# Kernel optimization log

Hardware: AMD Instinct MI355X
Metric: run time of the kernel (lower is better)

## Reference

```python
import jax, jax.numpy as jnp
import numpy as np

TOP_K = 8
N_EXPERTS = 64
ALPHA = 0.1
NORM_TOPK = True
SEQ_AUX = True


def setup_inputs() -> dict:
    key = jax.random.key(0)
    k1, k2 = jax.random.split(key)
    B, S, H = 4, 4096, 2048
    hidden_states = jax.random.normal(k1, (B, S, H), dtype=jnp.float32)
    # kaiming_uniform_(a=sqrt(5)) => bound = 1/sqrt(fan_in)
    bound = 1.0 / np.sqrt(H)
    weight = jax.random.uniform(k2, (N_EXPERTS, H), dtype=jnp.float32,
                                minval=-bound, maxval=bound)
    return {"hidden_states": hidden_states, "weight": weight}


def reference(hidden_states, weight):
    B, S, H = hidden_states.shape
    E, K = N_EXPERTS, TOP_K
    x = hidden_states.reshape(-1, H)                 # [T, H], T = B*S
    logits = jnp.einsum('th,eh->te', x, weight)      # gating GEMM
    scores = jax.nn.softmax(logits, axis=-1)         # [T, E]
    topk_weight, topk_idx = jax.lax.top_k(scores, K) # [T, K]
    if K > 1 and NORM_TOPK:
        topk_weight = topk_weight / (topk_weight.sum(-1, keepdims=True) + 1e-20)

    # batch-level load stats (bincount over selections)
    expert_loads = jnp.zeros((E,), jnp.float32).at[topk_idx.reshape(-1)].add(1.0)

    # sequence-level auxiliary load-balancing loss
    if SEQ_AUX:
        idx_b = topk_idx.reshape(B, S * K)           # [B, S*K]
        ce = jnp.zeros((B, E), jnp.float32)
        ce = ce.at[jnp.arange(B)[:, None], idx_b].add(1.0)
        ce = ce / (S * K / E)
        mean_scores = scores.reshape(B, S, E).mean(axis=1)   # [B, E]
        aux_loss = (ce * mean_scores).sum(axis=1).mean() * ALPHA
    else:
        ce = jax.nn.one_hot(topk_idx.reshape(-1), E).mean(0)
        Pi = scores.mean(0)
        aux_loss = (Pi * ce * E).sum() * ALPHA

    return (topk_idx, topk_weight, aux_loss, expert_loads)
```

## Files before the change

### kernel.cpp

```cpp
#include <hip/hip_runtime.h>
#include <hip/hip_bf16.h>
#include <math.h>

#define TOK 16384
#define HDIM 2048
#define NE 64
#define NB 4
#define KTOP 8
#define KC 64
#define NC (HDIM / KC)
#define BT 32

typedef __attribute__((ext_vector_type(8))) __bf16 bf16x8;
typedef __attribute__((ext_vector_type(4))) float f32x4;
typedef unsigned int uint;

__device__ __forceinline__ uint asu(float f) { union { float f; uint u; } c; c.f = f; return c.u; }
__device__ __forceinline__ float asf(uint u) { union { uint u; float f; } c; c.u = u; return c.f; }

__device__ __forceinline__ void split3(float v, uint& h, uint& m, uint& l) {
  uint u = asu(v);
  h = u & 0xffff0000u;
  float d = v - asf(h);
  m = asu(d) & 0xffff0000u;
  float d2 = d - asf(m);
  l = asu(d2);
}

__device__ __forceinline__ void split8(float4 a, float4 b,
                                       bf16x8& h8, bf16x8& m8, bf16x8& l8) {
  union { uint4 u; bf16x8 v; } H, M, L;
  uint h0, m0, l0, h1, m1, l1;
  split3(a.x, h0, m0, l0); split3(a.y, h1, m1, l1);
  H.u.x = (h0 >> 16) | (h1 & 0xffff0000u);
  M.u.x = (m0 >> 16) | (m1 & 0xffff0000u);
  L.u.x = (l0 >> 16) | (l1 & 0xffff0000u);
  split3(a.z, h0, m0, l0); split3(a.w, h1, m1, l1);
  H.u.y = (h0 >> 16) | (h1 & 0xffff0000u);
  M.u.y = (m0 >> 16) | (m1 & 0xffff0000u);
  L.u.y = (l0 >> 16) | (l1 & 0xffff0000u);
  split3(b.x, h0, m0, l0); split3(b.y, h1, m1, l1);
  H.u.z = (h0 >> 16) | (h1 & 0xffff0000u);
  M.u.z = (m0 >> 16) | (m1 & 0xffff0000u);
  L.u.z = (l0 >> 16) | (l1 & 0xffff0000u);
  split3(b.z, h0, m0, l0); split3(b.w, h1, m1, l1);
  H.u.w = (h0 >> 16) | (h1 & 0xffff0000u);
  M.u.w = (m0 >> 16) | (m1 & 0xffff0000u);
  L.u.w = (l0 >> 16) | (l1 & 0xffff0000u);
  h8 = H.v; m8 = M.v; l8 = L.v;
}

__device__ __forceinline__ void gl_lds16(const void* g, void* l) {
  __builtin_amdgcn_global_load_lds(
      (const __attribute__((address_space(1))) void*)g,
      (__attribute__((address_space(3))) void*)l, 16, 0, 0);
}

__global__ __launch_bounds__(256) void wsplit(const float* __restrict__ w,
                                              char* __restrict__ wpk,
                                              float* __restrict__ stats) {
  if (blockIdx.x == 0 && threadIdx.x < 128) {
    *(float4*)(stats + threadIdx.x * 4) = make_float4(0.f, 0.f, 0.f, 0.f);
  }
  int t = blockIdx.x * 256 + threadIdx.x;
  int lane = t & 63;
  int f2 = (t >> 6) & 1, half = (t >> 7) & 1, ks = (t >> 8) & 1, c = t >> 9;
  int e = half * 32 + f2 * 16 + (lane & 15);
  int k = c * 64 + ks * 32 + ((lane >> 4) << 3);
  const float* p = w + (size_t)e * HDIM + k;
  bf16x8 h8, m8, l8;
  split8(*(const float4*)p, *(const float4*)(p + 4), h8, m8, l8);
  union { bf16x8 v; uint4 u; } H, M, L;
  H.v = h8; M.v = m8; L.v = l8;
  size_t base = (size_t)c * 24576 + (size_t)ks * 12288 + (size_t)half * 6144
              + (size_t)f2 * 3072 + (size_t)lane * 16;
  *(uint4*)(wpk + base) = H.u;
  *(uint4*)(wpk + base + 1024) = M.u;
  *(uint4*)(wpk + base + 2048) = L.u;
}

__global__ __launch_bounds__(256, 2) void gate_fused(const float* __restrict__ x,
                                                     const char* __restrict__ wpk,
                                                     float* __restrict__ out,
                                                     float* __restrict__ ce,
                                                     float* __restrict__ ssum) {
  __shared__ __align__(16) char lds[65536];
  __shared__ float hist[NE];

  const int tid = threadIdx.x;
  const int bid = blockIdx.x;
  const int t0 = bid * BT;
  const int b = bid >> 7;
  const int lane = tid & 63;
  const int wid = tid >> 6;
  const int half = wid & 1;
  const int tg = (wid >> 1);

  if (tid < NE) hist[tid] = 0.f;

  const char* xsg[2];
  int xdo_[2];
#pragma unroll
  for (int r = 0; r < 2; ++r) {
    int s = r * 256 + tid;
    int stg = s >> 8, sks = (s >> 7) & 1, sq = (s >> 6) & 1, ln = s & 63;
    xsg[r] = (const char*)(x + (size_t)(t0 + stg * 16 + (ln & 15)) * HDIM
                           + sks * 32 + ((ln >> 4) << 3) + sq * 4);
    xdo_[r] = (r * 256 + wid * 64) * 16;
  }
  const char* wsrc = wpk + (size_t)lane * 16;

  f32x4 acc[2] = {{0.f, 0.f, 0.f, 0.f}, {0.f, 0.f, 0.f, 0.f}};

#define STAGE(cc, sel)                                                        \
  {                                                                           \
    char* wdst = lds + (sel) * 24576;                                         \
    const char* wp_ = wsrc + (size_t)(cc) * 24576;                            \
    _Pragma("unroll")                                                         \
    for (int i = 0; i < 6; ++i)                                               \
      gl_lds16(wp_ + (i * 4 + wid) * 1024, wdst + (i * 4 + wid) * 1024);      \
    char* xdst = lds + 49152 + (sel) * 8192;                                  \
    _Pragma("unroll")                                                         \
    for (int r = 0; r < 2; ++r)                                               \
      gl_lds16(xsg[r] + (size_t)(cc) * 256, xdst + xdo_[r]);                  \
  }

  STAGE(0, 0);
  asm volatile("s_waitcnt vmcnt(0)" ::: "memory");
  __builtin_amdgcn_s_barrier();
  asm volatile("" ::: "memory");

#pragma unroll 1
  for (int c = 0; c < NC; ++c) {
    const int sel = c & 1;
    if (c + 1 < NC) STAGE(c + 1, sel ^ 1);

    char* wb = lds + sel * 24576;
    char* xb = lds + 49152 + sel * 8192 + tg * 4096;
#pragma unroll
    for (int ks = 0; ks < 2; ++ks) {
      float4 X0 = *(const float4*)(xb + ks * 2048 + lane * 16);
      float4 X1 = *(const float4*)(xb + ks * 2048 + 1024 + lane * 16);
      bf16x8 ah, am, al;
      split8(X0, X1, ah, am, al);
      const char* wk = wb + ks * 12288 + half * 6144 + lane * 16;
#pragma unroll
      for (int f2 = 0; f2 < 2; ++f2) {
        const char* bb = wk + f2 * 3072;
        bf16x8 bh = *(const bf16x8*)(bb);
        bf16x8 bm = *(const bf16x8*)(bb + 1024);
        bf16x8 bl = *(const bf16x8*)(bb + 2048);
        acc[f2] = __builtin_amdgcn_mfma_f32_16x16x32_bf16(ah, bh, acc[f2], 0, 0, 0);
        acc[f2] = __builtin_amdgcn_mfma_f32_16x16x32_bf16(ah, bm, acc[f2], 0, 0, 0);
        acc[f2] = __builtin_amdgcn_mfma_f32_16x16x32_bf16(am, bh, acc[f2], 0, 0, 0);
        acc[f2] = __builtin_amdgcn_mfma_f32_16x16x32_bf16(ah, bl, acc[f2], 0, 0, 0);
        acc[f2] = __builtin_amdgcn_mfma_f32_16x16x32_bf16(al, bh, acc[f2], 0, 0, 0);
        acc[f2] = __builtin_amdgcn_mfma_f32_16x16x32_bf16(am, bm, acc[f2], 0, 0, 0);
      }
    }
    asm volatile("s_waitcnt vmcnt(0)" ::: "memory");
    __builtin_amdgcn_s_barrier();
    asm volatile("" ::: "memory");
  }
#undef STAGE

  float (*sc)[BT + 1] = (float(*)[BT + 1])lds;
#pragma unroll
  for (int f2 = 0; f2 < 2; ++f2) {
    int e = half * 32 + f2 * 16 + (lane & 15);
    int tk = tg * 16 + ((lane >> 4) << 2);
    sc[e][tk + 0] = acc[f2][0];
    sc[e][tk + 1] = acc[f2][1];
    sc[e][tk + 2] = acc[f2][2];
    sc[e][tk + 3] = acc[f2][3];
  }
  __syncthreads();

  const int t = tid >> 3;
  const int j = tid & 7;
  float p[8];
#pragma unroll
  for (int i = 0; i < 8; ++i) p[i] = sc[j * 8 + i][t];

  float m = p[0];
#pragma unroll
  for (int i = 1; i < 8; ++i) m = fmaxf(m, p[i]);
  m = fmaxf(m, __shfl_xor(m, 1, 8));
  m = fmaxf(m, __shfl_xor(m, 2, 8));
  m = fmaxf(m, __shfl_xor(m, 4, 8));
  float s = 0.f;
#pragma unroll
  for (int i = 0; i < 8; ++i) { p[i] = __expf(p[i] - m); s += p[i]; }
  s += __shfl_xor(s, 1, 8);
  s += __shfl_xor(s, 2, 8);
  s += __shfl_xor(s, 4, 8);
  float inv = 1.f / s;
#pragma unroll
  for (int i = 0; i < 8; ++i) { p[i] *= inv; sc[j * 8 + i][t] = p[i]; }

  unsigned used = 0;
  float wsum = 0.f;
  float wv[KTOP];
  int wi_[KTOP];
#pragma unroll
  for (int sel = 0; sel < KTOP; ++sel) {
    float bv = -1.f;
    int bi = 0;
#pragma unroll
    for (int i = 0; i < 8; ++i) {
      bool ok = !((used >> i) & 1u);
      if (ok && p[i] > bv) { bv = p[i]; bi = i; }
    }
    int ge = j * 8 + bi;
#pragma unroll
    for (int mk = 1; mk < 8; mk <<= 1) {
      float ov = __shfl_xor(bv, mk, 8);
      int og = __shfl_xor(ge, mk, 8);
      if (ov > bv || (ov == bv && og < ge)) { bv = ov; ge = og; }
    }
    if ((ge >> 3) == j) used |= 1u << (ge & 7);
    wv[sel] = bv;
    wi_[sel] = ge;
    wsum += bv;
  }
  if (j == 0) {
    float winv = 1.f / (wsum + 1e-20f);
#pragma unroll
    for (int sel = 0; sel < KTOP; ++sel) {
      out[(size_t)(t0 + t) * KTOP + sel] = (float)wi_[sel];
      out[(size_t)TOK * KTOP + (size_t)(t0 + t) * KTOP + sel] = wv[sel] * winv;
      atomicAdd(&hist[wi_[sel]], 1.f);
    }
  }
  __syncthreads();

  if (tid < NE) {
    float ssl = 0.f;
#pragma unroll
    for (int tt = 0; tt < BT; ++tt) ssl += sc[tid][tt];
    atomicAdd(&ssum[b * NE + tid], ssl);
    atomicAdd(&ce[b * NE + tid], hist[tid]);
  }
}

__global__ __launch_bounds__(64) void gate_final(const float* __restrict__ ce,
                                                 const float* __restrict__ ssum,
                                                 float* __restrict__ out) {
  const int e = threadIdx.x;
  float loads = 0.f, aux = 0.f;
#pragma unroll
  for (int b = 0; b < NB; ++b) {
    float c = ce[b * 64 + e];
    loads += c;
    aux += (c / 512.0f) * (ssum[b * 64 + e] / 4096.0f);
  }
  out[(size_t)2 * TOK * KTOP + 1 + e] = loads;
#pragma unroll
  for (int off = 32; off > 0; off >>= 1) aux += __shfl_down(aux, off);
  if (e == 0) out[(size_t)2 * TOK * KTOP] = aux * (0.1f / 4.0f);
}

extern "C" void kernel_launch(void* const* d_in, const int* in_sizes, int n_in,
                              void* d_out, int out_size, void* d_ws, size_t ws_size,
                              hipStream_t stream) {
  const float* x = (const float*)d_in[0];
  const float* w = (const float*)d_in[1];
  float* out = (float*)d_out;

  char* wpk = (char*)d_ws;
  float* ce = (float*)(wpk + (size_t)NC * 24576);
  float* ssum = ce + NB * NE;

  wsplit<<<dim3(64), dim3(256), 0, stream>>>(w, wpk, ce);
  gate_fused<<<dim3(TOK / BT), dim3(256), 0, stream>>>(x, wpk, out, ce, ssum);
  gate_final<<<dim3(1), dim3(64), 0, stream>>>(ce, ssum, out);
}
```

Baseline: 59.00 us.

## Widen gating tile to 64 tokens, stream x via registers, fuse final reduction

Doubles the token tile per block to 64 with 512 threads, so each staged weight chunk is reused across more tokens. K-steps now cover 128 columns. Activations are prefetched straight into registers in a double-buffered A/B scheme instead of passing through LDS. The separate finalize kernel is replaced by a last-block-done atomic counter inside the fused kernel, which removes one launch. The cost is higher register pressure, a 96KB LDS footprint that probably limits occupancy to one block per CU, and a grid of only 256 blocks.

```diff
diff --git a/kernel.cpp b/kernel.cpp
--- a/kernel.cpp
+++ b/kernel.cpp
@@ -7,9 +7,10 @@
 #define NE 64
 #define NB 4
 #define KTOP 8
-#define KC 64
-#define NC (HDIM / KC)
-#define BT 32
+#define KC2 128
+#define NSTEP (HDIM / KC2)
+#define NCH 32
+#define BT 64
 
 typedef __attribute__((ext_vector_type(8))) __bf16 bf16x8;
 typedef __attribute__((ext_vector_type(4))) float f32x4;
@@ -59,7 +60,7 @@
 __global__ __launch_bounds__(256) void wsplit(const float* __restrict__ w,
                                               char* __restrict__ wpk,
                                               float* __restrict__ stats) {
-  if (blockIdx.x == 0 && threadIdx.x < 128) {
+  if (blockIdx.x == 0 && threadIdx.x < 132) {
     *(float4*)(stats + threadIdx.x * 4) = make_float4(0.f, 0.f, 0.f, 0.f);
   }
   int t = blockIdx.x * 256 + threadIdx.x;
@@ -79,18 +80,20 @@
   *(uint4*)(wpk + base + 2048) = L.u;
 }
 
-__global__ __launch_bounds__(256, 2) void gate_fused(const float* __restrict__ x,
+__global__ __launch_bounds__(512, 2) void gate_fused(const float* __restrict__ x,
                                                      const char* __restrict__ wpk,
                                                      float* __restrict__ out,
                                                      float* __restrict__ ce,
-                                                     float* __restrict__ ssum) {
-  __shared__ __align__(16) char lds[65536];
+                                                     float* __restrict__ ssum,
+                                                     int* __restrict__ cnt) {
+  __shared__ __align__(16) char lds[98304];
   __shared__ float hist[NE];
+  __shared__ int lastflag;
 
   const int tid = threadIdx.x;
   const int bid = blockIdx.x;
   const int t0 = bid * BT;
-  const int b = bid >> 7;
+  const int b = bid >> 6;
   const int lane = tid & 63;
   const int wid = tid >> 6;
   const int half = wid & 1;
@@ -98,71 +101,82 @@
 
   if (tid < NE) hist[tid] = 0.f;
 
-  const char* xsg[2];
-  int xdo_[2];
-#pragma unroll
-  for (int r = 0; r < 2; ++r) {
-    int s = r * 256 + tid;
-    int stg = s >> 8, sks = (s >> 7) & 1, sq = (s >> 6) & 1, ln = s & 63;
-    xsg[r] = (const char*)(x + (size_t)(t0 + stg * 16 + (ln & 15)) * HDIM
-                           + sks * 32 + ((ln >> 4) << 3) + sq * 4);
-    xdo_[r] = (r * 256 + wid * 64) * 16;
-  }
+  const float* xrow = x + (size_t)(t0 + tg * 16 + (lane & 15)) * HDIM + ((lane >> 4) << 3);
   const char* wsrc = wpk + (size_t)lane * 16;
 
   f32x4 acc[2] = {{0.f, 0.f, 0.f, 0.f}, {0.f, 0.f, 0.f, 0.f}};
-
-#define STAGE(cc, sel)                                                        \
+  float4 XA[8], XB[8];
+
+#define STAGE_W(s, sel)                                                       \
   {                                                                           \
-    char* wdst = lds + (sel) * 24576;                                         \
-    const char* wp_ = wsrc + (size_t)(cc) * 24576;                            \
+    const char* wp_ = wsrc + (size_t)(s) * 49152;                             \
+    char* wd_ = lds + (sel) * 49152;                                          \
     _Pragma("unroll")                                                         \
     for (int i = 0; i < 6; ++i)                                               \
-      gl_lds16(wp_ + (i * 4 + wid) * 1024, wdst + (i * 4 + wid) * 1024);      \
-    char* xdst = lds + 49152 + (sel) * 8192;                                  \
+      gl_lds16(wp_ + (i * 8 + wid) * 1024, wd_ + (i * 8 + wid) * 1024);       \
+  }
+
+#define LOADX(XP, s)                                                          \
+  {                                                                           \
+    const float* xp_ = xrow + (size_t)(s) * KC2;                              \
+    XP[0] = *(const float4*)(xp_);                                            \
+    XP[1] = *(const float4*)(xp_ + 4);                                        \
+    XP[2] = *(const float4*)(xp_ + 32);                                       \
+    XP[3] = *(const float4*)(xp_ + 36);                                       \
+    XP[4] = *(const float4*)(xp_ + 64);                                       \
+    XP[5] = *(const float4*)(xp_ + 68);                                       \
+    XP[6] = *(const float4*)(xp_ + 96);                                       \
+    XP[7] = *(const float4*)(xp_ + 100);                                      \
+  }
+
+#define STEP(s, XU, XP)                                                       \
+  {                                                                           \
+    if ((s) + 1 < NSTEP) {                                                    \
+      STAGE_W((s) + 1, ((s) + 1) & 1);       \
+      LOADX(XP, (s) + 1);                         \
+    }                                                                         \
     _Pragma("unroll")                                                         \
-    for (int r = 0; r < 2; ++r)                                               \
-      gl_lds16(xsg[r] + (size_t)(cc) * 256, xdst + xdo_[r]);                  \
-  }
-
-  STAGE(0, 0);
+    for (int h = 0; h < 2; ++h) {                                             \
+      _Pragma("unroll")                                                       \
+      for (int ks = 0; ks < 2; ++ks) {                                        \
+        bf16x8 ah, am, al;                                                    \
+        split8(XU[h * 4 + ks * 2], XU[h * 4 + ks * 2 + 1], ah, am, al);       \
+        const char* wk = lds + ((s) & 1) * 49152 + h * 24576 + ks * 12288     \
+                       + half * 6144 + lane * 16;                             \
+        _Pragma("unroll")                                                     \
+        for (int f2 = 0; f2 < 2; ++f2) {                                      \
+          const char* bb = wk + f2 * 3072;                                    \
+          bf16x8 bh = *(const bf16x8*)(bb);                                   \
+          bf16x8 bm = *(const bf16x8*)(bb + 1024);                            \
+          bf16x8 bl = *(const bf16x8*)(bb + 2048);                            \
+          acc[f2] = __builtin_amdgcn_mfma_f32_16x16x32_bf16(ah, bh, acc[f2], 0, 0, 0); \
+          acc[f2] = __builtin_amdgcn_mfma_f32_16x16x32_bf16(ah, bm, acc[f2], 0, 0, 0); \
+          acc[f2] = __builtin_amdgcn_mfma_f32_16x16x32_bf16(am, bh, acc[f2], 0, 0, 0); \
+          acc[f2] = __builtin_amdgcn_mfma_f32_16x16x32_bf16(ah, bl, acc[f2], 0, 0, 0); \
+          acc[f2] = __builtin_amdgcn_mfma_f32_16x16x32_bf16(al, bh, acc[f2], 0, 0, 0); \
+          acc[f2] = __builtin_amdgcn_mfma_f32_16x16x32_bf16(am, bm, acc[f2], 0, 0, 0); \
+        }                                                                     \
+      }                                                                       \
+    }                                                                         \
+    asm volatile("s_waitcnt vmcnt(0)" ::: "memory");                          \
+    __builtin_amdgcn_s_barrier();                                             \
+    asm volatile("" ::: "memory");                                            \
+  }
+
+  STAGE_W(0, 0);
+  LOADX(XA, 0);
   asm volatile("s_waitcnt vmcnt(0)" ::: "memory");
   __builtin_amdgcn_s_barrier();
   asm volatile("" ::: "memory");
 
 #pragma unroll 1
-  for (int c = 0; c < NC; ++c) {
-    const int sel = c & 1;
-    if (c + 1 < NC) STAGE(c + 1, sel ^ 1);
-
-    char* wb = lds + sel * 24576;
-    char* xb = lds + 49152 + sel * 8192 + tg * 4096;
-#pragma unroll
-    for (int ks = 0; ks < 2; ++ks) {
-      float4 X0 = *(const float4*)(xb + ks * 2048 + lane * 16);
-      float4 X1 = *(const float4*)(xb + ks * 2048 + 1024 + lane * 16);
-      bf16x8 ah, am, al;
-      split8(X0, X1, ah, am, al);
-      const char* wk = wb + ks * 12288 + half * 6144 + lane * 16;
-#pragma unroll
-      for (int f2 = 0; f2 < 2; ++f2) {
-        const char* bb = wk + f2 * 3072;
-        bf16x8 bh = *(const bf16x8*)(bb);
-        bf16x8 bm = *(const bf16x8*)(bb + 1024);
-        bf16x8 bl = *(const bf16x8*)(bb + 2048);
-        acc[f2] = __builtin_amdgcn_mfma_f32_16x16x32_bf16(ah, bh, acc[f2], 0, 0, 0);
-        acc[f2] = __builtin_amdgcn_mfma_f32_16x16x32_bf16(ah, bm, acc[f2], 0, 0, 0);
-        acc[f2] = __builtin_amdgcn_mfma_f32_16x16x32_bf16(am, bh, acc[f2], 0, 0, 0);
-        acc[f2] = __builtin_amdgcn_mfma_f32_16x16x32_bf16(ah, bl, acc[f2], 0, 0, 0);
-        acc[f2] = __builtin_amdgcn_mfma_f32_16x16x32_bf16(al, bh, acc[f2], 0, 0, 0);
-        acc[f2] = __builtin_amdgcn_mfma_f32_16x16x32_bf16(am, bm, acc[f2], 0, 0, 0);
-      }
-    }
-    asm volatile("s_waitcnt vmcnt(0)" ::: "memory");
-    __builtin_amdgcn_s_barrier();
-    asm volatile("" ::: "memory");
-  }
-#undef STAGE
+  for (int ss = 0; ss < NSTEP; ss += 2) {
+    STEP(ss, XA, XB);
+    STEP(ss + 1, XB, XA);
+  }
+#undef STEP
+#undef STAGE_W
+#undef LOADX
 
   float (*sc)[BT + 1] = (float(*)[BT + 1])lds;
 #pragma unroll
@@ -241,23 +255,25 @@
     atomicAdd(&ssum[b * NE + tid], ssl);
     atomicAdd(&ce[b * NE + tid], hist[tid]);
   }
-}
-
-__global__ __launch_bounds__(64) void gate_final(const float* __restrict__ ce,
-                                                 const float* __restrict__ ssum,
-                                                 float* __restrict__ out) {
-  const int e = threadIdx.x;
-  float loads = 0.f, aux = 0.f;
-#pragma unroll
-  for (int b = 0; b < NB; ++b) {
-    float c = ce[b * 64 + e];
-    loads += c;
-    aux += (c / 512.0f) * (ssum[b * 64 + e] / 4096.0f);
-  }
-  out[(size_t)2 * TOK * KTOP + 1 + e] = loads;
-#pragma unroll
-  for (int off = 32; off > 0; off >>= 1) aux += __shfl_down(aux, off);
-  if (e == 0) out[(size_t)2 * TOK * KTOP] = aux * (0.1f / 4.0f);
+
+  __threadfence();
+  __syncthreads();
+  if (tid == 0) lastflag = (atomicAdd(cnt, 1) == gridDim.x - 1);
+  __syncthreads();
+  if (lastflag && tid < 64) {
+    const int e = tid;
+    float loads = 0.f, aux = 0.f;
+#pragma unroll
+    for (int b2 = 0; b2 < NB; ++b2) {
+      float c = ce[b2 * 64 + e];
+      loads += c;
+      aux += (c / 512.0f) * (ssum[b2 * 64 + e] / 4096.0f);
+    }
+    out[(size_t)2 * TOK * KTOP + 1 + e] = loads;
+#pragma unroll
+    for (int off = 32; off > 0; off >>= 1) aux += __shfl_down(aux, off);
+    if (e == 0) out[(size_t)2 * TOK * KTOP] = aux * (0.1f / 4.0f);
+  }
 }
 
 extern "C" void kernel_launch(void* const* d_in, const int* in_sizes, int n_in,
@@ -268,10 +284,10 @@
   float* out = (float*)d_out;
 
   char* wpk = (char*)d_ws;
-  float* ce = (float*)(wpk + (size_t)NC * 24576);
+  float* ce = (float*)(wpk + (size_t)NCH * 24576);
   float* ssum = ce + NB * NE;
+  int* cnt = (int*)(ssum + NB * NE);
 
   wsplit<<<dim3(64), dim3(256), 0, stream>>>(w, wpk, ce);
-  gate_fused<<<dim3(TOK / BT), dim3(256), 0, stream>>>(x, wpk, out, ce, ssum);
-  gate_final<<<dim3(1), dim3(64), 0, stream>>>(ce, ssum, out);
-}
+  gate_fused<<<dim3(TOK / BT), dim3(512), 0, stream>>>(x, wpk, out, ce, ssum, cnt);
+}
```

After: 101.1 us. +71.3%, slower.

## Stage raw fp32 weights, split in-kernel, and fold final reduction via last-block counter

Applied to the files above, without the earlier changes.

The weight prepack kernel now only reorders fp32 weights instead of pre-splitting them into three bf16 parts, and the main kernel splits the weights into hi/mid/lo in registers after loading from LDS. This shrinks per-chunk weight staging from 24 KB to 16 KB, lowering LDS use and global traffic per block. The separate final reduction kernel is removed; the last block to finish, detected through an atomic counter, computes the loads and aux loss. The cost is extra per-block ALU work for splitting the weights and an added fence plus atomic at the end of every block.

```diff
diff --git a/kernel.cpp b/kernel.cpp
--- a/kernel.cpp
+++ b/kernel.cpp
@@ -10,6 +10,7 @@
 #define KC 64
 #define NC (HDIM / KC)
 #define BT 32
+#define WCH 16384
 
 typedef __attribute__((ext_vector_type(8))) __bf16 bf16x8;
 typedef __attribute__((ext_vector_type(4))) float f32x4;
@@ -56,36 +57,31 @@
       (__attribute__((address_space(3))) void*)l, 16, 0, 0);
 }
 
-__global__ __launch_bounds__(256) void wsplit(const float* __restrict__ w,
-                                              char* __restrict__ wpk,
-                                              float* __restrict__ stats) {
-  if (blockIdx.x == 0 && threadIdx.x < 128) {
+__global__ __launch_bounds__(256) void wpack(const float* __restrict__ w,
+                                             char* __restrict__ wpk,
+                                             float* __restrict__ stats) {
+  if (blockIdx.x == 0 && threadIdx.x < 132) {
     *(float4*)(stats + threadIdx.x * 4) = make_float4(0.f, 0.f, 0.f, 0.f);
   }
   int t = blockIdx.x * 256 + threadIdx.x;
+  int c = t >> 10;
+  int g = (t >> 6) & 15;
   int lane = t & 63;
-  int f2 = (t >> 6) & 1, half = (t >> 7) & 1, ks = (t >> 8) & 1, c = t >> 9;
+  int ks = g >> 3, half = (g >> 2) & 1, f2 = (g >> 1) & 1, h16 = g & 1;
   int e = half * 32 + f2 * 16 + (lane & 15);
-  int k = c * 64 + ks * 32 + ((lane >> 4) << 3);
-  const float* p = w + (size_t)e * HDIM + k;
-  bf16x8 h8, m8, l8;
-  split8(*(const float4*)p, *(const float4*)(p + 4), h8, m8, l8);
-  union { bf16x8 v; uint4 u; } H, M, L;
-  H.v = h8; M.v = m8; L.v = l8;
-  size_t base = (size_t)c * 24576 + (size_t)ks * 12288 + (size_t)half * 6144
-              + (size_t)f2 * 3072 + (size_t)lane * 16;
-  *(uint4*)(wpk + base) = H.u;
-  *(uint4*)(wpk + base + 1024) = M.u;
-  *(uint4*)(wpk + base + 2048) = L.u;
+  int k = c * 64 + ks * 32 + ((lane >> 4) << 3) + h16 * 4;
+  *(uint4*)(wpk + (size_t)t * 16) = *(const uint4*)(w + (size_t)e * HDIM + k);
 }
 
 __global__ __launch_bounds__(256, 2) void gate_fused(const float* __restrict__ x,
                                                      const char* __restrict__ wpk,
                                                      float* __restrict__ out,
                                                      float* __restrict__ ce,
-                                                     float* __restrict__ ssum) {
-  __shared__ __align__(16) char lds[65536];
+                                                     float* __restrict__ ssum,
+                                                     int* __restrict__ cnt) {
+  __shared__ __align__(16) char lds[49152];
   __shared__ float hist[NE];
+  __shared__ int lastflag;
 
   const int tid = threadIdx.x;
   const int bid = blockIdx.x;
@@ -114,12 +110,12 @@
 
 #define STAGE(cc, sel)                                                        \
   {                                                                           \
-    char* wdst = lds + (sel) * 24576;                                         \
-    const char* wp_ = wsrc + (size_t)(cc) * 24576;                            \
+    const char* wp_ = wsrc + (size_t)(cc) * WCH;                              \
+    char* wd_ = lds + (sel) * WCH;                                            \
     _Pragma("unroll")                                                         \
-    for (int i = 0; i < 6; ++i)                                               \
-      gl_lds16(wp_ + (i * 4 + wid) * 1024, wdst + (i * 4 + wid) * 1024);      \
-    char* xdst = lds + 49152 + (sel) * 8192;                                  \
+    for (int r = 0; r < 4; ++r)                                               \
+      gl_lds16(wp_ + (r * 4 + wid) * 1024, wd_ + (r * 4 + wid) * 1024);       \
+    char* xdst = lds + 32768 + (sel) * 8192;                                  \
     _Pragma("unroll")                                                         \
     for (int r = 0; r < 2; ++r)                                               \
       gl_lds16(xsg[r] + (size_t)(cc) * 256, xdst + xdo_[r]);                  \
@@ -135,21 +131,21 @@
     const int sel = c & 1;
     if (c + 1 < NC) STAGE(c + 1, sel ^ 1);
 
-    char* wb = lds + sel * 24576;
-    char* xb = lds + 49152 + sel * 8192 + tg * 4096;
+    char* wb = lds + sel * WCH;
+    char* xb = lds + 32768 + sel * 8192 + tg * 4096;
 #pragma unroll
     for (int ks = 0; ks < 2; ++ks) {
       float4 X0 = *(const float4*)(xb + ks * 2048 + lane * 16);
       float4 X1 = *(const float4*)(xb + ks * 2048 + 1024 + lane * 16);
       bf16x8 ah, am, al;
       split8(X0, X1, ah, am, al);
-      const char* wk = wb + ks * 12288 + half * 6144 + lane * 16;
 #pragma unroll
       for (int f2 = 0; f2 < 2; ++f2) {
-        const char* bb = wk + f2 * 3072;
-        bf16x8 bh = *(const bf16x8*)(bb);
-        bf16x8 bm = *(const bf16x8*)(bb + 1024);
-        bf16x8 bl = *(const bf16x8*)(bb + 2048);
+        const int g = ks * 8 + half * 4 + f2 * 2;
+        float4 W0 = *(const float4*)(wb + g * 1024 + lane * 16);
+        float4 W1 = *(const float4*)(wb + (g + 1) * 1024 + lane * 16);
+        bf16x8 bh, bm, bl;
+        split8(W0, W1, bh, bm, bl);
         acc[f2] = __builtin_amdgcn_mfma_f32_16x16x32_bf16(ah, bh, acc[f2], 0, 0, 0);
         acc[f2] = __builtin_amdgcn_mfma_f32_16x16x32_bf16(ah, bm, acc[f2], 0, 0, 0);
         acc[f2] = __builtin_amdgcn_mfma_f32_16x16x32_bf16(am, bh, acc[f2], 0, 0, 0);
@@ -241,23 +237,26 @@
     atomicAdd(&ssum[b * NE + tid], ssl);
     atomicAdd(&ce[b * NE + tid], hist[tid]);
   }
-}
-
-__global__ __launch_bounds__(64) void gate_final(const float* __restrict__ ce,
-                                                 const float* __restrict__ ssum,
-                                                 float* __restrict__ out) {
-  const int e = threadIdx.x;
-  float loads = 0.f, aux = 0.f;
-#pragma unroll
-  for (int b = 0; b < NB; ++b) {
-    float c = ce[b * 64 + e];
-    loads += c;
-    aux += (c / 512.0f) * (ssum[b * 64 + e] / 4096.0f);
-  }
-  out[(size_t)2 * TOK * KTOP + 1 + e] = loads;
-#pragma unroll
-  for (int off = 32; off > 0; off >>= 1) aux += __shfl_down(aux, off);
-  if (e == 0) out[(size_t)2 * TOK * KTOP] = aux * (0.1f / 4.0f);
+
+  __threadfence();
+  __syncthreads();
+  if (tid == 0) lastflag = (atomicAdd(cnt, 1) == (int)gridDim.x - 1);
+  __syncthreads();
+  if (lastflag && tid < 64) {
+    const int e = tid;
+    float loads = 0.f, aux = 0.f;
+#pragma unroll
+    for (int b2 = 0; b2 < NB; ++b2) {
+      float cv = atomicAdd(&ce[b2 * 64 + e], 0.f);
+      float sv = atomicAdd(&ssum[b2 * 64 + e], 0.f);
+      loads += cv;
+      aux += (cv / 512.0f) * (sv / 4096.0f);
+    }
+    out[(size_t)2 * TOK * KTOP + 1 + e] = loads;
+#pragma unroll
+    for (int off = 32; off > 0; off >>= 1) aux += __shfl_down(aux, off);
+    if (e == 0) out[(size_t)2 * TOK * KTOP] = aux * (0.1f / 4.0f);
+  }
 }
 
 extern "C" void kernel_launch(void* const* d_in, const int* in_sizes, int n_in,
@@ -268,10 +267,10 @@
   float* out = (float*)d_out;
 
   char* wpk = (char*)d_ws;
-  float* ce = (float*)(wpk + (size_t)NC * 24576);
+  float* ce = (float*)(wpk + (size_t)NC * WCH);
   float* ssum = ce + NB * NE;
-
-  wsplit<<<dim3(64), dim3(256), 0, stream>>>(w, wpk, ce);
-  gate_fused<<<dim3(TOK / BT), dim3(256), 0, stream>>>(x, wpk, out, ce, ssum);
-  gate_final<<<dim3(1), dim3(64), 0, stream>>>(ce, ssum, out);
-}
+  int* cnt = (int*)(ssum + NB * NE);
+
+  wpack<<<dim3(128), dim3(256), 0, stream>>>(w, wpk, ce);
+  gate_fused<<<dim3(TOK / BT), dim3(256), 0, stream>>>(x, wpk, out, ce, ssum, cnt);
+}
```

Measured after the change: 119.4 us. +102.3%, slower.

## Double token tile per block and fold final reduction into last block

Applied to the files above, without the earlier changes.

Each block now handles 64 tokens with 512 threads instead of 32 tokens with 256, so every staged weight chunk in LDS is reused by twice as many tokens and the grid is half as large. The separate final kernel that combines the per-batch statistics is removed. Instead, a global counter picks the last finishing block, which computes the loads and the aux loss, saving one kernel launch. In exchange, LDS per block grows to 80KB, occupancy per CU drops, and the code now depends on a counter that wsplit zeroes on every call.

```diff
diff --git a/kernel.cpp b/kernel.cpp
--- a/kernel.cpp
+++ b/kernel.cpp
@@ -9,7 +9,7 @@
 #define KTOP 8
 #define KC 64
 #define NC (HDIM / KC)
-#define BT 32
+#define BT 64
 
 typedef __attribute__((ext_vector_type(8))) __bf16 bf16x8;
 typedef __attribute__((ext_vector_type(4))) float f32x4;
@@ -59,7 +59,7 @@
 __global__ __launch_bounds__(256) void wsplit(const float* __restrict__ w,
                                               char* __restrict__ wpk,
                                               float* __restrict__ stats) {
-  if (blockIdx.x == 0 && threadIdx.x < 128) {
+  if (blockIdx.x == 0 && threadIdx.x < 132) {
     *(float4*)(stats + threadIdx.x * 4) = make_float4(0.f, 0.f, 0.f, 0.f);
   }
   int t = blockIdx.x * 256 + threadIdx.x;
@@ -79,22 +79,24 @@
   *(uint4*)(wpk + base + 2048) = L.u;
 }
 
-__global__ __launch_bounds__(256, 2) void gate_fused(const float* __restrict__ x,
-                                                     const char* __restrict__ wpk,
-                                                     float* __restrict__ out,
-                                                     float* __restrict__ ce,
-                                                     float* __restrict__ ssum) {
-  __shared__ __align__(16) char lds[65536];
+__global__ __launch_bounds__(512) void gate_fused(const float* __restrict__ x,
+                                                  const char* __restrict__ wpk,
+                                                  float* __restrict__ out,
+                                                  float* __restrict__ ce,
+                                                  float* __restrict__ ssum,
+                                                  int* __restrict__ cnt) {
+  __shared__ __align__(16) char lds[81920];
   __shared__ float hist[NE];
+  __shared__ int lastflag;
 
   const int tid = threadIdx.x;
   const int bid = blockIdx.x;
   const int t0 = bid * BT;
-  const int b = bid >> 7;
+  const int b = bid >> 6;
   const int lane = tid & 63;
   const int wid = tid >> 6;
   const int half = wid & 1;
-  const int tg = (wid >> 1);
+  const int tg = wid >> 1;
 
   if (tid < NE) hist[tid] = 0.f;
 
@@ -102,11 +104,11 @@
   int xdo_[2];
 #pragma unroll
   for (int r = 0; r < 2; ++r) {
-    int s = r * 256 + tid;
+    int s = r * 512 + tid;
     int stg = s >> 8, sks = (s >> 7) & 1, sq = (s >> 6) & 1, ln = s & 63;
     xsg[r] = (const char*)(x + (size_t)(t0 + stg * 16 + (ln & 15)) * HDIM
                            + sks * 32 + ((ln >> 4) << 3) + sq * 4);
-    xdo_[r] = (r * 256 + wid * 64) * 16;
+    xdo_[r] = (r * 512 + wid * 64) * 16;
   }
   const char* wsrc = wpk + (size_t)lane * 16;
 
@@ -114,12 +116,12 @@
 
 #define STAGE(cc, sel)                                                        \
   {                                                                           \
-    char* wdst = lds + (sel) * 24576;                                         \
     const char* wp_ = wsrc + (size_t)(cc) * 24576;                            \
+    char* wd_ = lds + (sel) * 24576;                                          \
     _Pragma("unroll")                                                         \
-    for (int i = 0; i < 6; ++i)                                               \
-      gl_lds16(wp_ + (i * 4 + wid) * 1024, wdst + (i * 4 + wid) * 1024);      \
-    char* xdst = lds + 49152 + (sel) * 8192;                                  \
+    for (int i = 0; i < 3; ++i)                                               \
+      gl_lds16(wp_ + (i * 8 + wid) * 1024, wd_ + (i * 8 + wid) * 1024);       \
+    char* xdst = lds + 49152 + (sel) * 16384;                                 \
     _Pragma("unroll")                                                         \
     for (int r = 0; r < 2; ++r)                                               \
       gl_lds16(xsg[r] + (size_t)(cc) * 256, xdst + xdo_[r]);                  \
@@ -136,7 +138,7 @@
     if (c + 1 < NC) STAGE(c + 1, sel ^ 1);
 
     char* wb = lds + sel * 24576;
-    char* xb = lds + 49152 + sel * 8192 + tg * 4096;
+    char* xb = lds + 49152 + sel * 16384 + tg * 4096;
 #pragma unroll
     for (int ks = 0; ks < 2; ++ks) {
       float4 X0 = *(const float4*)(xb + ks * 2048 + lane * 16);
@@ -241,23 +243,26 @@
     atomicAdd(&ssum[b * NE + tid], ssl);
     atomicAdd(&ce[b * NE + tid], hist[tid]);
   }
-}
-
-__global__ __launch_bounds__(64) void gate_final(const float* __restrict__ ce,
-                                                 const float* __restrict__ ssum,
-                                                 float* __restrict__ out) {
-  const int e = threadIdx.x;
-  float loads = 0.f, aux = 0.f;
-#pragma unroll
-  for (int b = 0; b < NB; ++b) {
-    float c = ce[b * 64 + e];
-    loads += c;
-    aux += (c / 512.0f) * (ssum[b * 64 + e] / 4096.0f);
-  }
-  out[(size_t)2 * TOK * KTOP + 1 + e] = loads;
-#pragma unroll
-  for (int off = 32; off > 0; off >>= 1) aux += __shfl_down(aux, off);
-  if (e == 0) out[(size_t)2 * TOK * KTOP] = aux * (0.1f / 4.0f);
+
+  __threadfence();
+  __syncthreads();
+  if (tid == 0) lastflag = (atomicAdd(cnt, 1) == (int)gridDim.x - 1);
+  __syncthreads();
+  if (lastflag && tid < 64) {
+    const int e = tid;
+    float loads = 0.f, aux = 0.f;
+#pragma unroll
+    for (int b2 = 0; b2 < NB; ++b2) {
+      float cv = atomicAdd(&ce[b2 * 64 + e], 0.f);
+      float sv = atomicAdd(&ssum[b2 * 64 + e], 0.f);
+      loads += cv;
+      aux += (cv / 512.0f) * (sv / 4096.0f);
+    }
+    out[(size_t)2 * TOK * KTOP + 1 + e] = loads;
+#pragma unroll
+    for (int off = 32; off > 0; off >>= 1) aux += __shfl_down(aux, off);
+    if (e == 0) out[(size_t)2 * TOK * KTOP] = aux * (0.1f / 4.0f);
+  }
 }
 
 extern "C" void kernel_launch(void* const* d_in, const int* in_sizes, int n_in,
@@ -270,8 +275,8 @@
   char* wpk = (char*)d_ws;
   float* ce = (float*)(wpk + (size_t)NC * 24576);
   float* ssum = ce + NB * NE;
+  int* cnt = (int*)(ssum + NB * NE);
 
   wsplit<<<dim3(64), dim3(256), 0, stream>>>(w, wpk, ce);
-  gate_fused<<<dim3(TOK / BT), dim3(256), 0, stream>>>(x, wpk, out, ce, ssum);
-  gate_final<<<dim3(1), dim3(64), 0, stream>>>(ce, ssum, out);
-}
+  gate_fused<<<dim3(TOK / BT), dim3(512), 0, stream>>>(x, wpk, out, ce, ssum, cnt);
+}
```

After: 93.66 us. 1.59x slower.
